# Optimization experiments

Measured on AMD Instinct MI355X. Metric: run time of the kernel, lower is better.

The kernel has to match this reference:

```python
import jax, jax.numpy as jnp
import numpy as np

B, Q, C, H, W, CH = 16, 1024, 256, 32, 32, 8  # batch, queries, dim, grid, conv hidden


def setup_inputs() -> dict:
    key = jax.random.key(0)
    ks = jax.random.split(key, 8)
    return {
        "queries": jax.random.normal(ks[0], (B, Q, C), jnp.float32),
        "keys": jax.random.normal(ks[1], (B, H, W, C), jnp.float32),
        "pos": jax.random.randint(ks[2], (B, Q, 2), 0, H, dtype=jnp.int32),
        "rel_bias": jax.random.normal(ks[3], (2 * H - 1, 2 * W - 1), jnp.float32) * 0.02,
        "conv1_weight": jax.random.normal(ks[4], (CH, 1, 3, 3), jnp.float32) * 0.1,
        "conv1_bias": jnp.zeros((CH,), jnp.float32),
        "conv2_weight": jax.random.normal(ks[5], (1, CH, 3, 3), jnp.float32) * 0.1,
        "conv2_bias": jnp.zeros((1,), jnp.float32),
    }


def reference(queries, keys, pos, rel_bias, conv1_weight, conv1_bias, conv2_weight, conv2_bias):
    Bq, Qn, Cd = queries.shape
    _, Hh, Ww, _ = keys.shape
    # fused relative-grid attention scores: [B,Q,H,W]
    scores = jnp.einsum('bqc,bhwc->bqhw', queries, keys) / jnp.sqrt(jnp.float32(Cd))
    dh = jnp.arange(Hh)[None, None, :] - pos[..., 0][..., None] + (Hh - 1)  # [B,Q,H]
    dw = jnp.arange(Ww)[None, None, :] - pos[..., 1][..., None] + (Ww - 1)  # [B,Q,W]
    bias = rel_bias[dh[..., :, None], dw[..., None, :]]                     # [B,Q,H,W]
    attn = jax.nn.softmax((scores + bias).reshape(Bq, Qn, Hh * Ww), axis=-1)
    attn = attn.reshape(Bq, Qn, Hh, Ww)
    # residual conv block on each (1,H,W) attention map
    x = attn.reshape(Bq * Qn, 1, Hh, Ww)
    dn = ('NCHW', 'OIHW', 'NCHW')
    h = jax.lax.conv_general_dilated(x, conv1_weight, (1, 1), 'SAME', dimension_numbers=dn)
    h = jax.nn.relu(h + conv1_bias[None, :, None, None])
    h = jax.lax.conv_general_dilated(h, conv2_weight, (1, 1), 'SAME', dimension_numbers=dn)
    h = h + conv2_bias[None, :, None, None]
    return (x + h).reshape(Bq, Qn, Hh, Ww)
```

## Files before the change

kernel.cpp:

```cpp
#include <hip/hip_runtime.h>

typedef _Float16 h2 __attribute__((ext_vector_type(2)));
typedef _Float16 h8 __attribute__((ext_vector_type(8)));
typedef float f32x4 __attribute__((ext_vector_type(4)));

#define B_  16
#define Q_  1024
#define C_  256
#define HW_ 1024
#define TQA 32
#define NTA 512
#define QLD 264
#define BT  256
#define IPB 4
#define XRB 80
#define XIMGB (34 * XRB)
#define HRB 576

__device__ __forceinline__ h2 u2h(unsigned u) { return __builtin_bit_cast(h2, u); }
__device__ __forceinline__ unsigned h2u(h2 h) { return __builtin_bit_cast(unsigned, h); }

__device__ __forceinline__ float fdot2f(h2 a, h2 b, float c) {
#if __has_builtin(__builtin_amdgcn_fdot2)
    return __builtin_amdgcn_fdot2(a, b, c, false);
#else
    return c + (float)a[0] * (float)b[0] + (float)a[1] * (float)b[1];
#endif
}
__device__ __forceinline__ float dotw(unsigned x, unsigned w, float acc) {
    return fdot2f(u2h(x), u2h(w), acc);
}

__global__ void cvt_keys_f16(const float* __restrict__ src,
                             _Float16* __restrict__ dst, int n8) {
    int i = blockIdx.x * blockDim.x + threadIdx.x;
    if (i >= n8) return;
    const float4* s = (const float4*)src;
    float4 a = s[2 * i], b = s[2 * i + 1];
    h8 v;
    v[0] = (_Float16)a.x; v[1] = (_Float16)a.y; v[2] = (_Float16)a.z; v[3] = (_Float16)a.w;
    v[4] = (_Float16)b.x; v[5] = (_Float16)b.y; v[6] = (_Float16)b.z; v[7] = (_Float16)b.w;
    *(h8*)(dst + (size_t)i * 8) = v;
}

__global__ void pack_weights(const float* __restrict__ w1, const float* __restrict__ b1,
                             const float* __restrict__ w2, const float* __restrict__ b2,
                             unsigned* __restrict__ wpk) {
    int t = threadIdx.x;
    if (t < 24) {
        int ch = t / 3, dy = t - ch * 3;
        h2 v = {(_Float16)w1[ch * 9 + dy * 3 + 0], (_Float16)w1[ch * 9 + dy * 3 + 1]};
        wpk[t] = h2u(v);
    } else if (t < 48) {
        int i = t - 24; int ch = i / 3, dy = i - ch * 3;
        h2 v = {(_Float16)w1[ch * 9 + dy * 3 + 2], (_Float16)0.f};
        wpk[t] = h2u(v);
    } else if (t < 56) {
        wpk[t] = __builtin_bit_cast(unsigned, b1[t - 48]);
    } else if (t < 92) {
        int i = t - 56; int t9 = i >> 2, c2 = i & 3;
        h2 v = {(_Float16)w2[(2 * c2) * 9 + t9], (_Float16)w2[(2 * c2 + 1) * 9 + t9]};
        wpk[t] = h2u(v);
    } else if (t == 92) {
        wpk[t] = __builtin_bit_cast(unsigned, b2[0]);
    }
}

__global__ __launch_bounds__(NTA, 4) void attn_kernel(
    const float* __restrict__ queries, const _Float16* __restrict__ keysh,
    const int* __restrict__ pos, const float* __restrict__ rel_bias,
    _Float16* __restrict__ xmapg)
{
    __shared__ _Float16 q_lds[TQA * QLD];
    __shared__ _Float16 bias_lds[63 * 64];
    __shared__ float red_max[8][TQA];
    __shared__ float red_sum[8][TQA];
    __shared__ int2  pos_lds[TQA];

    const int tid = threadIdx.x;
    const int bid = blockIdx.x;
    const int swz = (bid & 7) * 64 + (bid >> 3);
    const int batch = swz >> 5;
    const int tile  = swz & 31;

    {
        const float4* qsrc = (const float4*)(queries + (size_t)(batch * Q_ + tile * TQA) * C_);
        #pragma unroll
        for (int i = 0; i < 4; ++i) {
            int e4 = i * NTA + tid;
            float4 v = qsrc[e4];
            int row = e4 >> 6, col4 = e4 & 63;
            _Float16* d = &q_lds[row * QLD + col4 * 4];
            d[0] = (_Float16)v.x; d[1] = (_Float16)v.y;
            d[2] = (_Float16)v.z; d[3] = (_Float16)v.w;
        }
        for (int idx = tid; idx < 63 * 63; idx += NTA) {
            int r = idx / 63;
            bias_lds[r * 64 + (idx - r * 63)] = (_Float16)rel_bias[idx];
        }
        if (tid < TQA)
            pos_lds[tid] = ((const int2*)pos)[batch * Q_ + tile * TQA + tid];
    }
    __syncthreads();

    const int lane = tid & 63;
    const int wv   = tid >> 6;
    const int kgrp = (lane >> 4) * 8;
    const int l15  = lane & 15;
    const int rowbase = (lane >> 4) << 2;

    f32x4 acc0[8], acc1[8];
    #pragma unroll
    for (int f = 0; f < 8; ++f) {
        acc0[f] = f32x4{0.f, 0.f, 0.f, 0.f};
        acc1[f] = f32x4{0.f, 0.f, 0.f, 0.f};
    }

    const _Float16* kb = keysh + (size_t)batch * (HW_ * C_)
                       + (size_t)(wv * 128 + l15) * C_ + kgrp;
    #pragma unroll
    for (int ks = 0; ks < 8; ++ks) {
        h8 a0 = *(const h8*)&q_lds[l15 * QLD + ks * 32 + kgrp];
        h8 a1 = *(const h8*)&q_lds[(16 + l15) * QLD + ks * 32 + kgrp];
        #pragma unroll
        for (int f = 0; f < 8; ++f) {
            h8 bfr = *(const h8*)(kb + f * (16 * C_) + ks * 32);
            acc0[f] = __builtin_amdgcn_mfma_f32_16x16x32_f16(a0, bfr, acc0[f], 0, 0, 0);
            acc1[f] = __builtin_amdgcn_mfma_f32_16x16x32_f16(a1, bfr, acc1[f], 0, 0, 0);
        }
    }

    int p0r[2][4], p1r[2][4];
    #pragma unroll
    for (int mt = 0; mt < 2; ++mt)
        #pragma unroll
        for (int r = 0; r < 4; ++r) {
            int2 pp = pos_lds[mt * 16 + rowbase + r];
            p0r[mt][r] = pp.x; p1r[mt][r] = pp.y;
        }

    float mrow[2][4];
    #pragma unroll
    for (int mt = 0; mt < 2; ++mt)
        #pragma unroll
        for (int r = 0; r < 4; ++r) mrow[mt][r] = -3e38f;

    #pragma unroll
    for (int f = 0; f < 8; ++f) {
        int col = wv * 128 + f * 16 + l15;
        int hh = col >> 5, ww = col & 31;
        #pragma unroll
        for (int r = 0; r < 4; ++r) {
            float s0 = acc0[f][r] * 0.0625f
                     + (float)bias_lds[(hh - p0r[0][r] + 31) * 64 + (ww - p1r[0][r] + 31)];
            acc0[f][r] = s0;
            mrow[0][r] = fmaxf(mrow[0][r], s0);
            float s1 = acc1[f][r] * 0.0625f
                     + (float)bias_lds[(hh - p0r[1][r] + 31) * 64 + (ww - p1r[1][r] + 31)];
            acc1[f][r] = s1;
            mrow[1][r] = fmaxf(mrow[1][r], s1);
        }
    }
    #pragma unroll
    for (int mt = 0; mt < 2; ++mt)
        #pragma unroll
        for (int r = 0; r < 4; ++r) {
            float m = mrow[mt][r];
            m = fmaxf(m, __shfl_xor(m, 1, 64));
            m = fmaxf(m, __shfl_xor(m, 2, 64));
            m = fmaxf(m, __shfl_xor(m, 4, 64));
            m = fmaxf(m, __shfl_xor(m, 8, 64));
            mrow[mt][r] = m;
        }
    if (l15 == 0) {
        #pragma unroll
        for (int mt = 0; mt < 2; ++mt)
            #pragma unroll
            for (int r = 0; r < 4; ++r)
                red_max[wv][mt * 16 + rowbase + r] = mrow[mt][r];
    }
    __syncthreads();

    float M4[2][4];
    #pragma unroll
    for (int mt = 0; mt < 2; ++mt)
        #pragma unroll
        for (int r = 0; r < 4; ++r) {
            float m = red_max[0][mt * 16 + rowbase + r];
            #pragma unroll
            for (int w = 1; w < 8; ++w) m = fmaxf(m, red_max[w][mt * 16 + rowbase + r]);
            M4[mt][r] = m;
        }

    float sm[2][4];
    #pragma unroll
    for (int mt = 0; mt < 2; ++mt)
        #pragma unroll
        for (int r = 0; r < 4; ++r) sm[mt][r] = 0.f;
    #pragma unroll
    for (int f = 0; f < 8; ++f) {
        #pragma unroll
        for (int r = 0; r < 4; ++r) {
            float e0 = __expf(acc0[f][r] - M4[0][r]);
            acc0[f][r] = e0; sm[0][r] += e0;
            float e1 = __expf(acc1[f][r] - M4[1][r]);
            acc1[f][r] = e1; sm[1][r] += e1;
        }
    }
    #pragma unroll
    for (int mt = 0; mt < 2; ++mt)
        #pragma unroll
        for (int r = 0; r < 4; ++r) {
            float s = sm[mt][r];
            s += __shfl_xor(s, 1, 64);
            s += __shfl_xor(s, 2, 64);
            s += __shfl_xor(s, 4, 64);
            s += __shfl_xor(s, 8, 64);
            sm[mt][r] = s;
        }
    if (l15 == 0) {
        #pragma unroll
        for (int mt = 0; mt < 2; ++mt)
            #pragma unroll
            for (int r = 0; r < 4; ++r)
                red_sum[wv][mt * 16 + rowbase + r] = sm[mt][r];
    }
    __syncthreads();

    float sinv[2][4];
    #pragma unroll
    for (int mt = 0; mt < 2; ++mt)
        #pragma unroll
        for (int r = 0; r < 4; ++r) {
            float S = red_sum[0][mt * 16 + rowbase + r];
            #pragma unroll
            for (int w = 1; w < 8; ++w) S += red_sum[w][mt * 16 + rowbase + r];
            sinv[mt][r] = 1.0f / S;
        }

    _Float16* xg = xmapg + (size_t)(batch * Q_ + tile * TQA) * HW_;
    #pragma unroll
    for (int f = 0; f < 8; ++f) {
        int col = wv * 128 + f * 16 + l15;
        #pragma unroll
        for (int r = 0; r < 4; ++r) {
            xg[(size_t)(rowbase + r) * HW_ + col] = (_Float16)(acc0[f][r] * sinv[0][r]);
            xg[(size_t)(16 + rowbase + r) * HW_ + col] = (_Float16)(acc1[f][r] * sinv[1][r]);
        }
    }
}

__global__ __launch_bounds__(BT, 4) void conv_kernel(
    const _Float16* __restrict__ xmapg, const unsigned* __restrict__ wpk,
    float* __restrict__ out)
{
    __shared__ __align__(16) char xall[16 + IPB * XIMGB];
    __shared__ __align__(16) char Hb[34 * HRB];
    __shared__ unsigned wsh[56];

    const int tid = threadIdx.x;
    const int bid = blockIdx.x;
    const int swz = (bid & 7) * 512 + (bid >> 3);
    const size_t img0 = (size_t)swz * IPB;

    {
        const uint4 z = uint4{0u, 0u, 0u, 0u};
        uint4* xz = (uint4*)xall;
        for (int i = tid; i < (int)sizeof(xall) / 16; i += BT) xz[i] = z;
        uint4* hz = (uint4*)Hb;
        for (int i = tid; i < (int)sizeof(Hb) / 16; i += BT) hz[i] = z;
    }
    if (tid < 56) wsh[tid] = wpk[tid];
    __syncthreads();

    #pragma unroll
    for (int i = 0; i < 2; ++i) {
        int c = i * BT + tid;
        int im = c >> 7, cc = c & 127, r = cc >> 2, q = cc & 3;
        uint4 v = *(const uint4*)(xmapg + img0 * HW_ + (size_t)im * HW_ + cc * 8);
        *(uint4*)(xall + 16 + im * XIMGB + (r + 1) * XRB + q * 16) = v;
    }

    unsigned wA[8][3], wB[8][3];
    float b1r[8];
    #pragma unroll
    for (int ch = 0; ch < 8; ++ch) {
        b1r[ch] = __builtin_bit_cast(float, wsh[48 + ch]);
        #pragma unroll
        for (int dy = 0; dy < 3; ++dy) {
            wA[ch][dy] = wsh[ch * 3 + dy];
            wB[ch][dy] = wsh[24 + ch * 3 + dy];
        }
    }
    unsigned w2s[9][4];
    #pragma unroll
    for (int t = 0; t < 9; ++t)
        #pragma unroll
        for (int c2 = 0; c2 < 4; ++c2) w2s[t][c2] = wpk[56 + t * 4 + c2];
    const float b2r = __builtin_bit_cast(float, wpk[92]);

    const int m4 = tid & 7;
    const int y  = tid >> 3;
    const int x0 = m4 << 2;

    const char* const xb  = xall + 16 + y * XRB + 2 * x0;
    char* const hwr = Hb + (y + 1) * HRB + m4 * 16;
    const char* const hrd = Hb + y * HRB + m4 * 16;

    __syncthreads();

    #pragma unroll 1
    for (int img = 0; img < IPB; ++img) {
        const char* xi = xb + img * XIMGB;

        unsigned Pm[3], Pc[3], Pe[3], A0[3], A1[3], E4[3];
        #pragma unroll
        for (int dy = 0; dy < 3; ++dy) {
            unsigned pv = *(const unsigned*)(xi + dy * XRB - 4);
            uint2 a01   = *(const uint2*)(xi + dy * XRB);
            unsigned e4 = *(const unsigned*)(xi + dy * XRB + 8);
            A0[dy] = a01.x; A1[dy] = a01.y; E4[dy] = e4;
            Pm[dy] = __builtin_amdgcn_alignbit(a01.x, pv, 16);
            Pc[dy] = __builtin_amdgcn_alignbit(a01.y, a01.x, 16);
            Pe[dy] = __builtin_amdgcn_alignbit(e4, a01.y, 16);
        }

        unsigned hvw[4][4];
        #pragma unroll
        for (int p = 0; p < 4; ++p) {
            const int cA = 2 * p, cB = 2 * p + 1;
            float sA[4], sB[4];
            #pragma unroll
            for (int j = 0; j < 4; ++j) { sA[j] = b1r[cA]; sB[j] = b1r[cB]; }
            #pragma unroll
            for (int dy = 0; dy < 3; ++dy) {
                sA[0] = dotw(Pm[dy], wA[cA][dy], sA[0]);
                sA[0] = dotw(Pc[dy], wB[cA][dy], sA[0]);
                sA[1] = dotw(A0[dy], wA[cA][dy], sA[1]);
                sA[1] = dotw(A1[dy], wB[cA][dy], sA[1]);
                sA[2] = dotw(Pc[dy], wA[cA][dy], sA[2]);
                sA[2] = dotw(Pe[dy], wB[cA][dy], sA[2]);
                sA[3] = dotw(A1[dy], wA[cA][dy], sA[3]);
                sA[3] = dotw(E4[dy], wB[cA][dy], sA[3]);
                sB[0] = dotw(Pm[dy], wA[cB][dy], sB[0]);
                sB[0] = dotw(Pc[dy], wB[cB][dy], sB[0]);
                sB[1] = dotw(A0[dy], wA[cB][dy], sB[1]);
                sB[1] = dotw(A1[dy], wB[cB][dy], sB[1]);
                sB[2] = dotw(Pc[dy], wA[cB][dy], sB[2]);
                sB[2] = dotw(Pe[dy], wB[cB][dy], sB[2]);
                sB[3] = dotw(A1[dy], wA[cB][dy], sB[3]);
                sB[3] = dotw(E4[dy], wB[cB][dy], sB[3]);
            }
            #pragma unroll
            for (int j = 0; j < 4; ++j) {
                h2 r;
                r[0] = (_Float16)fmaxf(sA[j], 0.f);
                r[1] = (_Float16)fmaxf(sB[j], 0.f);
                hvw[j][p] = h2u(r);
            }
        }

        __syncthreads();

        {
            *(uint4*)(hwr + 144) = uint4{hvw[0][0], hvw[0][1], hvw[0][2], hvw[0][3]};
            *(uint4*)(hwr + 288) = uint4{hvw[1][0], hvw[1][1], hvw[1][2], hvw[1][3]};
            *(uint4*)(hwr + 432) = uint4{hvw[2][0], hvw[2][1], hvw[2][2], hvw[2][3]};
            *(uint4*)(hwr + 16)  = uint4{hvw[3][0], hvw[3][1], hvw[3][2], hvw[3][3]};
        }
        __syncthreads();

        float a2[4] = {b2r, b2r, b2r, b2r};
        #pragma unroll
        for (int dy = 0; dy < 3; ++dy) {
            const char* rb = hrd + dy * HRB;
            uint4 Hv[6];
            Hv[0] = *(const uint4*)(rb + 0);
            Hv[1] = *(const uint4*)(rb + 144);
            Hv[2] = *(const uint4*)(rb + 288);
            Hv[3] = *(const uint4*)(rb + 432);
            Hv[4] = *(const uint4*)(rb + 16);
            Hv[5] = *(const uint4*)(rb + 160);
            #pragma unroll
            for (int j = 0; j < 4; ++j) {
                #pragma unroll
                for (int dx = 0; dx < 3; ++dx) {
                    const int tt = dy * 3 + dx;
                    const uint4 uu = Hv[j + dx];
                    a2[j] = dotw(uu.x, w2s[tt][0], a2[j]);
                    a2[j] = dotw(uu.y, w2s[tt][1], a2[j]);
                    a2[j] = dotw(uu.z, w2s[tt][2], a2[j]);
                    a2[j] = dotw(uu.w, w2s[tt][3], a2[j]);
                }
            }
        }
        {
            h2 lo = u2h(A0[1]), hi = u2h(A1[1]);
            float4 o;
            o.x = (float)lo[0] + a2[0];
            o.y = (float)lo[1] + a2[1];
            o.z = (float)hi[0] + a2[2];
            o.w = (float)hi[1] + a2[3];
            *(float4*)(out + (img0 + img) * HW_ + y * 32 + x0) = o;
        }
    }
}

extern "C" void kernel_launch(void* const* d_in, const int* in_sizes, int n_in,
                              void* d_out, int out_size, void* d_ws, size_t ws_size,
                              hipStream_t stream) {
    const float* queries  = (const float*)d_in[0];
    const float* keys     = (const float*)d_in[1];
    const int*   pos      = (const int*)d_in[2];
    const float* rel_bias = (const float*)d_in[3];
    const float* w1       = (const float*)d_in[4];
    const float* b1       = (const float*)d_in[5];
    const float* w2       = (const float*)d_in[6];
    const float* b2       = (const float*)d_in[7];
    float* out = (float*)d_out;

    unsigned*  wpk   = (unsigned*)d_ws;
    _Float16*  keysh = (_Float16*)((char*)d_ws + 4096);
    _Float16*  xmapg = (_Float16*)((char*)d_ws + 4096 + 8388608);

    const int n8 = (B_ * HW_ * C_) / 8;
    pack_weights<<<dim3(1), dim3(128), 0, stream>>>(w1, b1, w2, b2, wpk);
    cvt_keys_f16<<<dim3(n8 / 256), dim3(256), 0, stream>>>(keys, keysh, n8);
    attn_kernel<<<dim3(B_ * (Q_ / TQA)), dim3(NTA), 0, stream>>>(
        queries, keysh, pos, rel_bias, xmapg);
    conv_kernel<<<dim3((B_ * Q_) / IPB), dim3(BT), 0, stream>>>(xmapg, wpk, out);
}
```

Before: 115.8 us.

## Double query tile in attention and move conv math to packed fp32

```diff
diff --git a/kernel.cpp b/kernel.cpp
--- a/kernel.cpp
+++ b/kernel.cpp
@@ -3,32 +3,25 @@
 typedef _Float16 h2 __attribute__((ext_vector_type(2)));
 typedef _Float16 h8 __attribute__((ext_vector_type(8)));
 typedef float f32x4 __attribute__((ext_vector_type(4)));
+typedef float f2 __attribute__((ext_vector_type(2)));
 
 #define B_  16
 #define Q_  1024
 #define C_  256
 #define HW_ 1024
-#define TQA 32
+#define TQA 64
 #define NTA 512
 #define QLD 264
 #define BT  256
-#define IPB 4
 #define XRB 80
 #define XIMGB (34 * XRB)
 #define HRB 576
+#define HBIMG (34 * HRB)
 
 __device__ __forceinline__ h2 u2h(unsigned u) { return __builtin_bit_cast(h2, u); }
 __device__ __forceinline__ unsigned h2u(h2 h) { return __builtin_bit_cast(unsigned, h); }
-
-__device__ __forceinline__ float fdot2f(h2 a, h2 b, float c) {
-#if __has_builtin(__builtin_amdgcn_fdot2)
-    return __builtin_amdgcn_fdot2(a, b, c, false);
-#else
-    return c + (float)a[0] * (float)b[0] + (float)a[1] * (float)b[1];
-#endif
-}
-__device__ __forceinline__ float dotw(unsigned x, unsigned w, float acc) {
-    return fdot2f(u2h(x), u2h(w), acc);
+__device__ __forceinline__ unsigned pkrtz(float a, float b) {
+    return __builtin_bit_cast(unsigned, __builtin_amdgcn_cvt_pkrtz(a, b));
 }
 
 __global__ void cvt_keys_f16(const float* __restrict__ src,
@@ -45,28 +38,26 @@
 
 __global__ void pack_weights(const float* __restrict__ w1, const float* __restrict__ b1,
                              const float* __restrict__ w2, const float* __restrict__ b2,
-                             unsigned* __restrict__ wpk) {
+                             float* __restrict__ wpkf) {
     int t = threadIdx.x;
-    if (t < 24) {
-        int ch = t / 3, dy = t - ch * 3;
-        h2 v = {(_Float16)w1[ch * 9 + dy * 3 + 0], (_Float16)w1[ch * 9 + dy * 3 + 1]};
-        wpk[t] = h2u(v);
-    } else if (t < 48) {
-        int i = t - 24; int ch = i / 3, dy = i - ch * 3;
-        h2 v = {(_Float16)w1[ch * 9 + dy * 3 + 2], (_Float16)0.f};
-        wpk[t] = h2u(v);
-    } else if (t < 56) {
-        wpk[t] = __builtin_bit_cast(unsigned, b1[t - 48]);
-    } else if (t < 92) {
-        int i = t - 56; int t9 = i >> 2, c2 = i & 3;
-        h2 v = {(_Float16)w2[(2 * c2) * 9 + t9], (_Float16)w2[(2 * c2 + 1) * 9 + t9]};
-        wpk[t] = h2u(v);
-    } else if (t == 92) {
-        wpk[t] = __builtin_bit_cast(unsigned, b2[0]);
-    }
-}
-
-__global__ __launch_bounds__(NTA, 4) void attn_kernel(
+    if (t < 36) {
+        int tt = t >> 2, p = t & 3;
+        wpkf[2 * t + 0] = w1[(2 * p) * 9 + tt];
+        wpkf[2 * t + 1] = w1[(2 * p + 1) * 9 + tt];
+    } else if (t < 40) {
+        int p = t - 36;
+        wpkf[72 + 2 * p + 0] = b1[2 * p];
+        wpkf[72 + 2 * p + 1] = b1[2 * p + 1];
+    } else if (t < 76) {
+        int i = t - 40; int tt = i >> 2, p = i & 3;
+        wpkf[80 + 2 * i + 0] = w2[(2 * p) * 9 + tt];
+        wpkf[80 + 2 * i + 1] = w2[(2 * p + 1) * 9 + tt];
+    } else if (t == 76) {
+        wpkf[152] = b2[0];
+    }
+}
+
+__global__ __launch_bounds__(NTA, 2) void attn_kernel(
     const float* __restrict__ queries, const _Float16* __restrict__ keysh,
     const int* __restrict__ pos, const float* __restrict__ rel_bias,
     _Float16* __restrict__ xmapg)
@@ -79,14 +70,14 @@
 
     const int tid = threadIdx.x;
     const int bid = blockIdx.x;
-    const int swz = (bid & 7) * 64 + (bid >> 3);
-    const int batch = swz >> 5;
-    const int tile  = swz & 31;
+    const int swz = (bid & 7) * 32 + (bid >> 3);
+    const int batch = swz >> 4;
+    const int tile  = swz & 15;
 
     {
         const float4* qsrc = (const float4*)(queries + (size_t)(batch * Q_ + tile * TQA) * C_);
         #pragma unroll
-        for (int i = 0; i < 4; ++i) {
+        for (int i = 0; i < 8; ++i) {
             int e4 = i * NTA + tid;
             float4 v = qsrc[e4];
             int row = e4 >> 6, col4 = e4 & 63;
@@ -109,39 +100,41 @@
     const int l15  = lane & 15;
     const int rowbase = (lane >> 4) << 2;
 
-    f32x4 acc0[8], acc1[8];
-    #pragma unroll
-    for (int f = 0; f < 8; ++f) {
-        acc0[f] = f32x4{0.f, 0.f, 0.f, 0.f};
-        acc1[f] = f32x4{0.f, 0.f, 0.f, 0.f};
-    }
+    f32x4 acc[4][8];
+    #pragma unroll
+    for (int mt = 0; mt < 4; ++mt)
+        #pragma unroll
+        for (int f = 0; f < 8; ++f) acc[mt][f] = f32x4{0.f, 0.f, 0.f, 0.f};
 
     const _Float16* kb = keysh + (size_t)batch * (HW_ * C_)
                        + (size_t)(wv * 128 + l15) * C_ + kgrp;
     #pragma unroll
     for (int ks = 0; ks < 8; ++ks) {
-        h8 a0 = *(const h8*)&q_lds[l15 * QLD + ks * 32 + kgrp];
-        h8 a1 = *(const h8*)&q_lds[(16 + l15) * QLD + ks * 32 + kgrp];
+        h8 a[4];
+        #pragma unroll
+        for (int mt = 0; mt < 4; ++mt)
+            a[mt] = *(const h8*)&q_lds[(mt * 16 + l15) * QLD + ks * 32 + kgrp];
         #pragma unroll
         for (int f = 0; f < 8; ++f) {
             h8 bfr = *(const h8*)(kb + f * (16 * C_) + ks * 32);
-            acc0[f] = __builtin_amdgcn_mfma_f32_16x16x32_f16(a0, bfr, acc0[f], 0, 0, 0);
-            acc1[f] = __builtin_amdgcn_mfma_f32_16x16x32_f16(a1, bfr, acc1[f], 0, 0, 0);
-        }
-    }
-
-    int p0r[2][4], p1r[2][4];
-    #pragma unroll
-    for (int mt = 0; mt < 2; ++mt)
+            #pragma unroll
+            for (int mt = 0; mt < 4; ++mt)
+                acc[mt][f] = __builtin_amdgcn_mfma_f32_16x16x32_f16(a[mt], bfr, acc[mt][f], 0, 0, 0);
+        }
+    }
+
+    int p0r[4][4], p1r[4][4];
+    #pragma unroll
+    for (int mt = 0; mt < 4; ++mt)
         #pragma unroll
         for (int r = 0; r < 4; ++r) {
             int2 pp = pos_lds[mt * 16 + rowbase + r];
             p0r[mt][r] = pp.x; p1r[mt][r] = pp.y;
         }
 
-    float mrow[2][4];
-    #pragma unroll
-    for (int mt = 0; mt < 2; ++mt)
+    float mrow[4][4];
+    #pragma unroll
+    for (int mt = 0; mt < 4; ++mt)
         #pragma unroll
         for (int r = 0; r < 4; ++r) mrow[mt][r] = -3e38f;
 
@@ -150,19 +143,17 @@
         int col = wv * 128 + f * 16 + l15;
         int hh = col >> 5, ww = col & 31;
         #pragma unroll
-        for (int r = 0; r < 4; ++r) {
-            float s0 = acc0[f][r] * 0.0625f
-                     + (float)bias_lds[(hh - p0r[0][r] + 31) * 64 + (ww - p1r[0][r] + 31)];
-            acc0[f][r] = s0;
-            mrow[0][r] = fmaxf(mrow[0][r], s0);
-            float s1 = acc1[f][r] * 0.0625f
-                     + (float)bias_lds[(hh - p0r[1][r] + 31) * 64 + (ww - p1r[1][r] + 31)];
-            acc1[f][r] = s1;
-            mrow[1][r] = fmaxf(mrow[1][r], s1);
-        }
-    }
-    #pragma unroll
-    for (int mt = 0; mt < 2; ++mt)
+        for (int mt = 0; mt < 4; ++mt)
+            #pragma unroll
+            for (int r = 0; r < 4; ++r) {
+                float s = acc[mt][f][r] * 0.0625f
+                        + (float)bias_lds[(hh - p0r[mt][r] + 31) * 64 + (ww - p1r[mt][r] + 31)];
+                acc[mt][f][r] = s;
+                mrow[mt][r] = fmaxf(mrow[mt][r], s);
+            }
+    }
+    #pragma unroll
+    for (int mt = 0; mt < 4; ++mt)
         #pragma unroll
         for (int r = 0; r < 4; ++r) {
             float m = mrow[mt][r];
@@ -174,41 +165,38 @@
         }
     if (l15 == 0) {
         #pragma unroll
-        for (int mt = 0; mt < 2; ++mt)
+        for (int mt = 0; mt < 4; ++mt)
             #pragma unroll
             for (int r = 0; r < 4; ++r)
                 red_max[wv][mt * 16 + rowbase + r] = mrow[mt][r];
     }
     __syncthreads();
 
-    float M4[2][4];
-    #pragma unroll
-    for (int mt = 0; mt < 2; ++mt)
+    float sm[4][4];
+    #pragma unroll
+    for (int mt = 0; mt < 4; ++mt)
         #pragma unroll
         for (int r = 0; r < 4; ++r) {
             float m = red_max[0][mt * 16 + rowbase + r];
             #pragma unroll
             for (int w = 1; w < 8; ++w) m = fmaxf(m, red_max[w][mt * 16 + rowbase + r]);
-            M4[mt][r] = m;
-        }
-
-    float sm[2][4];
-    #pragma unroll
-    for (int mt = 0; mt < 2; ++mt)
-        #pragma unroll
-        for (int r = 0; r < 4; ++r) sm[mt][r] = 0.f;
+            mrow[mt][r] = m;
+            sm[mt][r] = 0.f;
+        }
+
     #pragma unroll
     for (int f = 0; f < 8; ++f) {
         #pragma unroll
-        for (int r = 0; r < 4; ++r) {
-            float e0 = __expf(acc0[f][r] - M4[0][r]);
-            acc0[f][r] = e0; sm[0][r] += e0;
-            float e1 = __expf(acc1[f][r] - M4[1][r]);
-            acc1[f][r] = e1; sm[1][r] += e1;
-        }
-    }
-    #pragma unroll
-    for (int mt = 0; mt < 2; ++mt)
+        for (int mt = 0; mt < 4; ++mt)
+            #pragma unroll
+            for (int r = 0; r < 4; ++r) {
+                float e = __expf(acc[mt][f][r] - mrow[mt][r]);
+                acc[mt][f][r] = e;
+                sm[mt][r] += e;
+            }
+    }
+    #pragma unroll
+    for (int mt = 0; mt < 4; ++mt)
         #pragma unroll
         for (int r = 0; r < 4; ++r) {
             float s = sm[mt][r];
@@ -220,48 +208,46 @@
         }
     if (l15 == 0) {
         #pragma unroll
-        for (int mt = 0; mt < 2; ++mt)
+        for (int mt = 0; mt < 4; ++mt)
             #pragma unroll
             for (int r = 0; r < 4; ++r)
                 red_sum[wv][mt * 16 + rowbase + r] = sm[mt][r];
     }
     __syncthreads();
 
-    float sinv[2][4];
-    #pragma unroll
-    for (int mt = 0; mt < 2; ++mt)
+    _Float16* xg = xmapg + (size_t)(batch * Q_ + tile * TQA) * HW_;
+    #pragma unroll
+    for (int mt = 0; mt < 4; ++mt) {
+        float sinv[4];
         #pragma unroll
         for (int r = 0; r < 4; ++r) {
             float S = red_sum[0][mt * 16 + rowbase + r];
             #pragma unroll
             for (int w = 1; w < 8; ++w) S += red_sum[w][mt * 16 + rowbase + r];
-            sinv[mt][r] = 1.0f / S;
-        }
-
-    _Float16* xg = xmapg + (size_t)(batch * Q_ + tile * TQA) * HW_;
-    #pragma unroll
-    for (int f = 0; f < 8; ++f) {
-        int col = wv * 128 + f * 16 + l15;
-        #pragma unroll
-        for (int r = 0; r < 4; ++r) {
-            xg[(size_t)(rowbase + r) * HW_ + col] = (_Float16)(acc0[f][r] * sinv[0][r]);
-            xg[(size_t)(16 + rowbase + r) * HW_ + col] = (_Float16)(acc1[f][r] * sinv[1][r]);
-        }
-    }
-}
-
-__global__ __launch_bounds__(BT, 4) void conv_kernel(
-    const _Float16* __restrict__ xmapg, const unsigned* __restrict__ wpk,
+            sinv[r] = 1.0f / S;
+        }
+        #pragma unroll
+        for (int f = 0; f < 8; ++f) {
+            int col = wv * 128 + f * 16 + l15;
+            #pragma unroll
+            for (int r = 0; r < 4; ++r)
+                xg[(size_t)(mt * 16 + rowbase + r) * HW_ + col]
+                    = (_Float16)(acc[mt][f][r] * sinv[r]);
+        }
+    }
+}
+
+__global__ __launch_bounds__(BT, 3) void conv_kernel(
+    const _Float16* __restrict__ xmapg, const float* __restrict__ wpkf,
     float* __restrict__ out)
 {
-    __shared__ __align__(16) char xall[16 + IPB * XIMGB];
-    __shared__ __align__(16) char Hb[34 * HRB];
-    __shared__ unsigned wsh[56];
+    __shared__ __align__(16) char xall[16 + 4 * XIMGB];
+    __shared__ __align__(16) char Hb[2 * HBIMG];
 
     const int tid = threadIdx.x;
     const int bid = blockIdx.x;
     const int swz = (bid & 7) * 512 + (bid >> 3);
-    const size_t img0 = (size_t)swz * IPB;
+    const size_t img0 = (size_t)swz * 4;
 
     {
         const uint4 z = uint4{0u, 0u, 0u, 0u};
@@ -270,7 +256,6 @@
         uint4* hz = (uint4*)Hb;
         for (int i = tid; i < (int)sizeof(Hb) / 16; i += BT) hz[i] = z;
     }
-    if (tid < 56) wsh[tid] = wpk[tid];
     __syncthreads();
 
     #pragma unroll
@@ -281,128 +266,121 @@
         *(uint4*)(xall + 16 + im * XIMGB + (r + 1) * XRB + q * 16) = v;
     }
 
-    unsigned wA[8][3], wB[8][3];
-    float b1r[8];
-    #pragma unroll
-    for (int ch = 0; ch < 8; ++ch) {
-        b1r[ch] = __builtin_bit_cast(float, wsh[48 + ch]);
+    f2 w1v[9][4], b1v[4], w2v[9][4];
+    #pragma unroll
+    for (int t = 0; t < 9; ++t)
+        #pragma unroll
+        for (int p = 0; p < 4; ++p) {
+            w1v[t][p] = f2{wpkf[(t * 4 + p) * 2], wpkf[(t * 4 + p) * 2 + 1]};
+            w2v[t][p] = f2{wpkf[80 + (t * 4 + p) * 2], wpkf[80 + (t * 4 + p) * 2 + 1]};
+        }
+    #pragma unroll
+    for (int p = 0; p < 4; ++p)
+        b1v[p] = f2{wpkf[72 + 2 * p], wpkf[72 + 2 * p + 1]};
+    const float b2r = wpkf[152];
+
+    const int r4   = tid & 3;
+    const int y    = (tid >> 2) & 31;
+    const int half = tid >> 7;
+    const int x0   = r4 << 3;
+
+    const char* const xrow0 = xall + 16 + y * XRB + x0 * 2;
+    char* const hb = Hb + half * HBIMG;
+    char* const hst = hb + (y + 1) * HRB;
+    const char* const hrd = hb + y * HRB + r4 * 32;
+
+    __syncthreads();
+
+    #pragma unroll 1
+    for (int pass = 0; pass < 2; ++pass) {
+        const int img = pass * 2 + half;
+        const char* xi = xrow0 + img * XIMGB;
+
+        float xf[3][10];
         #pragma unroll
         for (int dy = 0; dy < 3; ++dy) {
-            wA[ch][dy] = wsh[ch * 3 + dy];
-            wB[ch][dy] = wsh[24 + ch * 3 + dy];
-        }
-    }
-    unsigned w2s[9][4];
-    #pragma unroll
-    for (int t = 0; t < 9; ++t)
-        #pragma unroll
-        for (int c2 = 0; c2 < 4; ++c2) w2s[t][c2] = wpk[56 + t * 4 + c2];
-    const float b2r = __builtin_bit_cast(float, wpk[92]);
-
-    const int m4 = tid & 7;
-    const int y  = tid >> 3;
-    const int x0 = m4 << 2;
-
-    const char* const xb  = xall + 16 + y * XRB + 2 * x0;
-    char* const hwr = Hb + (y + 1) * HRB + m4 * 16;
-    const char* const hrd = Hb + y * HRB + m4 * 16;
-
-    __syncthreads();
-
-    #pragma unroll 1
-    for (int img = 0; img < IPB; ++img) {
-        const char* xi = xb + img * XIMGB;
-
-        unsigned Pm[3], Pc[3], Pe[3], A0[3], A1[3], E4[3];
-        #pragma unroll
-        for (int dy = 0; dy < 3; ++dy) {
-            unsigned pv = *(const unsigned*)(xi + dy * XRB - 4);
-            uint2 a01   = *(const uint2*)(xi + dy * XRB);
-            unsigned e4 = *(const unsigned*)(xi + dy * XRB + 8);
-            A0[dy] = a01.x; A1[dy] = a01.y; E4[dy] = e4;
-            Pm[dy] = __builtin_amdgcn_alignbit(a01.x, pv, 16);
-            Pc[dy] = __builtin_amdgcn_alignbit(a01.y, a01.x, 16);
-            Pe[dy] = __builtin_amdgcn_alignbit(e4, a01.y, 16);
-        }
-
-        unsigned hvw[4][4];
-        #pragma unroll
-        for (int p = 0; p < 4; ++p) {
-            const int cA = 2 * p, cB = 2 * p + 1;
-            float sA[4], sB[4];
-            #pragma unroll
-            for (int j = 0; j < 4; ++j) { sA[j] = b1r[cA]; sB[j] = b1r[cB]; }
+            unsigned em = *(const unsigned*)(xi + dy * XRB - 4);
+            uint4 a07   = *(const uint4*)(xi + dy * XRB);
+            unsigned e8 = *(const unsigned*)(xi + dy * XRB + 16);
+            xf[dy][0] = (float)u2h(em)[1];
+            xf[dy][1] = (float)u2h(a07.x)[0]; xf[dy][2] = (float)u2h(a07.x)[1];
+            xf[dy][3] = (float)u2h(a07.y)[0]; xf[dy][4] = (float)u2h(a07.y)[1];
+            xf[dy][5] = (float)u2h(a07.z)[0]; xf[dy][6] = (float)u2h(a07.z)[1];
+            xf[dy][7] = (float)u2h(a07.w)[0]; xf[dy][8] = (float)u2h(a07.w)[1];
+            xf[dy][9] = (float)u2h(e8)[0];
+        }
+
+        #pragma unroll
+        for (int j2 = 0; j2 < 4; ++j2) {
+            f2 accA[4], accB[4];
+            #pragma unroll
+            for (int p = 0; p < 4; ++p) { accA[p] = b1v[p]; accB[p] = b1v[p]; }
             #pragma unroll
             for (int dy = 0; dy < 3; ++dy) {
-                sA[0] = dotw(Pm[dy], wA[cA][dy], sA[0]);
-                sA[0] = dotw(Pc[dy], wB[cA][dy], sA[0]);
-                sA[1] = dotw(A0[dy], wA[cA][dy], sA[1]);
-                sA[1] = dotw(A1[dy], wB[cA][dy], sA[1]);
-                sA[2] = dotw(Pc[dy], wA[cA][dy], sA[2]);
-                sA[2] = dotw(Pe[dy], wB[cA][dy], sA[2]);
-                sA[3] = dotw(A1[dy], wA[cA][dy], sA[3]);
-                sA[3] = dotw(E4[dy], wB[cA][dy], sA[3]);
-                sB[0] = dotw(Pm[dy], wA[cB][dy], sB[0]);
-                sB[0] = dotw(Pc[dy], wB[cB][dy], sB[0]);
-                sB[1] = dotw(A0[dy], wA[cB][dy], sB[1]);
-                sB[1] = dotw(A1[dy], wB[cB][dy], sB[1]);
-                sB[2] = dotw(Pc[dy], wA[cB][dy], sB[2]);
-                sB[2] = dotw(Pe[dy], wB[cB][dy], sB[2]);
-                sB[3] = dotw(A1[dy], wA[cB][dy], sB[3]);
-                sB[3] = dotw(E4[dy], wB[cB][dy], sB[3]);
+                const float* xr = xf[dy];
+                f2 s0 = {xr[2 * j2 + 0], xr[2 * j2 + 0]};
+                f2 s1 = {xr[2 * j2 + 1], xr[2 * j2 + 1]};
+                f2 s2 = {xr[2 * j2 + 2], xr[2 * j2 + 2]};
+                f2 s3 = {xr[2 * j2 + 3], xr[2 * j2 + 3]};
+                #pragma unroll
+                for (int p = 0; p < 4; ++p) {
+                    accA[p] += s0 * w1v[dy * 3 + 0][p];
+                    accA[p] += s1 * w1v[dy * 3 + 1][p];
+                    accA[p] += s2 * w1v[dy * 3 + 2][p];
+                    accB[p] += s1 * w1v[dy * 3 + 0][p];
+                    accB[p] += s2 * w1v[dy * 3 + 1][p];
+                    accB[p] += s3 * w1v[dy * 3 + 2][p];
+                }
             }
-            #pragma unroll
-            for (int j = 0; j < 4; ++j) {
-                h2 r;
-                r[0] = (_Float16)fmaxf(sA[j], 0.f);
-                r[1] = (_Float16)fmaxf(sB[j], 0.f);
-                hvw[j][p] = h2u(r);
+            uint4 hvA, hvB;
+            #pragma unroll
+            for (int p = 0; p < 4; ++p) {
+                ((unsigned*)&hvA)[p] = pkrtz(fmaxf(accA[p][0], 0.f), fmaxf(accA[p][1], 0.f));
+                ((unsigned*)&hvB)[p] = pkrtz(fmaxf(accB[p][0], 0.f), fmaxf(accB[p][1], 0.f));
             }
-        }
-
+            const int cpA = x0 + 2 * j2 + 1, cpB = cpA + 1;
+            *(uint4*)(hst + ((cpA & 3) * 9 + (cpA >> 2)) * 16) = hvA;
+            *(uint4*)(hst + ((cpB & 3) * 9 + (cpB >> 2)) * 16) = hvB;
+        }
         __syncthreads();
 
-        {
-            *(uint4*)(hwr + 144) = uint4{hvw[0][0], hvw[0][1], hvw[0][2], hvw[0][3]};
-            *(uint4*)(hwr + 288) = uint4{hvw[1][0], hvw[1][1], hvw[1][2], hvw[1][3]};
-            *(uint4*)(hwr + 432) = uint4{hvw[2][0], hvw[2][1], hvw[2][2], hvw[2][3]};
-            *(uint4*)(hwr + 16)  = uint4{hvw[3][0], hvw[3][1], hvw[3][2], hvw[3][3]};
-        }
-        __syncthreads();
-
-        float a2[4] = {b2r, b2r, b2r, b2r};
+        f2 a2[8];
+        #pragma unroll
+        for (int j = 0; j < 8; ++j) a2[j] = f2{0.f, 0.f};
         #pragma unroll
         for (int dy = 0; dy < 3; ++dy) {
             const char* rb = hrd + dy * HRB;
-            uint4 Hv[6];
-            Hv[0] = *(const uint4*)(rb + 0);
-            Hv[1] = *(const uint4*)(rb + 144);
-            Hv[2] = *(const uint4*)(rb + 288);
-            Hv[3] = *(const uint4*)(rb + 432);
-            Hv[4] = *(const uint4*)(rb + 16);
-            Hv[5] = *(const uint4*)(rb + 160);
-            #pragma unroll
-            for (int j = 0; j < 4; ++j) {
+            uint4 Hv[10];
+            Hv[0] = *(const uint4*)(rb + 0);    Hv[1] = *(const uint4*)(rb + 144);
+            Hv[2] = *(const uint4*)(rb + 288);  Hv[3] = *(const uint4*)(rb + 432);
+            Hv[4] = *(const uint4*)(rb + 16);   Hv[5] = *(const uint4*)(rb + 160);
+            Hv[6] = *(const uint4*)(rb + 304);  Hv[7] = *(const uint4*)(rb + 448);
+            Hv[8] = *(const uint4*)(rb + 32);   Hv[9] = *(const uint4*)(rb + 176);
+            #pragma unroll
+            for (int k = 0; k < 10; ++k) {
                 #pragma unroll
-                for (int dx = 0; dx < 3; ++dx) {
-                    const int tt = dy * 3 + dx;
-                    const uint4 uu = Hv[j + dx];
-                    a2[j] = dotw(uu.x, w2s[tt][0], a2[j]);
-                    a2[j] = dotw(uu.y, w2s[tt][1], a2[j]);
-                    a2[j] = dotw(uu.z, w2s[tt][2], a2[j]);
-                    a2[j] = dotw(uu.w, w2s[tt][3], a2[j]);
+                for (int p = 0; p < 4; ++p) {
+                    h2 hv = u2h(((const unsigned*)&Hv[k])[p]);
+                    f2 hf = {(float)hv[0], (float)hv[1]};
+                    #pragma unroll
+                    for (int dx = 0; dx < 3; ++dx) {
+                        const int j = k - dx;
+                        if (j >= 0 && j < 8)
+                            a2[j] += hf * w2v[dy * 3 + dx][p];
+                    }
                 }
             }
         }
         {
-            h2 lo = u2h(A0[1]), hi = u2h(A1[1]);
-            float4 o;
-            o.x = (float)lo[0] + a2[0];
-            o.y = (float)lo[1] + a2[1];
-            o.z = (float)hi[0] + a2[2];
-            o.w = (float)hi[1] + a2[3];
-            *(float4*)(out + (img0 + img) * HW_ + y * 32 + x0) = o;
-        }
+            float o[8];
+            #pragma unroll
+            for (int j = 0; j < 8; ++j)
+                o[j] = xf[1][j + 1] + a2[j][0] + a2[j][1] + b2r;
+            float* op = out + (img0 + img) * HW_ + y * 32 + x0;
+            *(float4*)(op)     = float4{o[0], o[1], o[2], o[3]};
+            *(float4*)(op + 4) = float4{o[4], o[5], o[6], o[7]};
+        }
+        __syncthreads();
     }
 }
 
@@ -419,14 +397,14 @@
     const float* b2       = (const float*)d_in[7];
     float* out = (float*)d_out;
 
-    unsigned*  wpk   = (unsigned*)d_ws;
+    float*     wpkf  = (float*)d_ws;
     _Float16*  keysh = (_Float16*)((char*)d_ws + 4096);
     _Float16*  xmapg = (_Float16*)((char*)d_ws + 4096 + 8388608);
 
     const int n8 = (B_ * HW_ * C_) / 8;
-    pack_weights<<<dim3(1), dim3(128), 0, stream>>>(w1, b1, w2, b2, wpk);
+    pack_weights<<<dim3(1), dim3(128), 0, stream>>>(w1, b1, w2, b2, wpkf);
     cvt_keys_f16<<<dim3(n8 / 256), dim3(256), 0, stream>>>(keys, keysh, n8);
     attn_kernel<<<dim3(B_ * (Q_ / TQA)), dim3(NTA), 0, stream>>>(
         queries, keysh, pos, rel_bias, xmapg);
-    conv_kernel<<<dim3((B_ * Q_) / IPB), dim3(BT), 0, stream>>>(xmapg, wpk, out);
-}
+    conv_kernel<<<dim3((B_ * Q_) / 4), dim3(BT), 0, stream>>>(xmapg, wpkf, out);
+}
```

New measurement: 121.3 us. 1.05x slower.
